# Optimization experiments

Measured on AMD Instinct MI355X. Metric: run time of the kernel, lower is better.

## Reference

```python
import jax, jax.numpy as jnp
import numpy as np

IMG = 8       # image_size
LH = 150      # l_h
LQ = 10       # l_q
K = 10        # value-iteration steps
B = 16384     # batch
N_STATES = 2 + IMG * IMG


def _conv(x, w, pad):
    # NCHW conv, stride 1
    return jax.lax.conv_general_dilated(
        x, w, window_strides=(1, 1), padding=[(pad, pad), (pad, pad)],
        dimension_numbers=('NCHW', 'OIHW', 'NCHW'))


def setup_inputs() -> dict:
    key = jax.random.key(0)
    ks = jax.random.split(key, 8)
    grid = jax.random.normal(ks[0], (B, IMG * IMG), dtype=jnp.float32)
    pos = jax.random.randint(ks[1], (B, 2), 0, IMG).astype(jnp.float32)
    S = jnp.concatenate([grid, pos], axis=1)                      # [B, 66]
    Wh = jax.random.normal(ks[2], (LH, 1, 3, 3), jnp.float32) * 0.1
    bh = jnp.zeros((LH,), jnp.float32)
    Wr = jax.random.normal(ks[3], (1, LH, 1, 1), jnp.float32) * 0.1
    Wq = jax.random.normal(ks[4], (LQ, 1, 3, 3), jnp.float32) * 0.1
    w = jax.random.normal(ks[5], (LQ, 1, 3, 3), jnp.float32) * 0.1
    Wfc = jax.random.normal(ks[6], (8, LQ), jnp.float32) * 0.1
    return {'S': S, 'Wh': Wh, 'bh': bh, 'Wr': Wr, 'Wq': Wq, 'w': w, 'Wfc': Wfc}


def reference(S, Wh, bh, Wr, Wq, w, Wfc):
    X = S[:, :IMG * IMG].reshape(-1, 1, IMG, IMG)                 # [B,1,8,8]
    s1 = S[:, IMG * IMG].astype(jnp.int32)                        # row index
    s2 = S[:, IMG * IMG + 1].astype(jnp.int32)                    # col index

    h = _conv(X, Wh, 1) + bh[None, :, None, None]                 # [B,150,8,8]
    r = _conv(h, Wr, 0)                                           # [B,1,8,8]
    q = _conv(r, Wq, 1)                                           # [B,10,8,8]
    v = jnp.max(q, axis=1, keepdims=True)                         # [B,1,8,8]

    Wcat = jnp.concatenate([Wq, w], axis=1)                       # [10,2,3,3]

    def step(v, _):
        qq = _conv(jnp.concatenate([r, v], axis=1), Wcat, 1)
        return jnp.max(qq, axis=1, keepdims=True), None

    v, _ = jax.lax.scan(step, v, None, length=K - 1)
    q = _conv(jnp.concatenate([r, v], axis=1), Wcat, 1)           # [B,10,8,8]

    bidx = jnp.arange(q.shape[0])
    q_sel = q[bidx, :, s1, s2]                                    # [B,10]
    logits = q_sel @ Wfc.T                                        # [B,8]
    return logits
```

## Files before the change

### kernel.cpp

```cpp
#include <hip/hip_runtime.h>

#define IMG 8
#define LH 150
#define LQ 10
#define KITER 10
#define ROW (IMG * IMG + 2)

__device__ __forceinline__ float bperm(int byte_addr, float v) {
    return __builtin_bit_cast(float,
        __builtin_amdgcn_ds_bpermute(byte_addr, __builtin_bit_cast(int, v)));
}

__device__ __forceinline__ float rfl(float v) {
    return __builtin_bit_cast(float,
        __builtin_amdgcn_readfirstlane(__builtin_bit_cast(int, v)));
}

__device__ __forceinline__ float swz24(float v) {
    return __builtin_bit_cast(float,
        __builtin_amdgcn_ds_swizzle(__builtin_bit_cast(int, v), 0x601F));
}

template <int CTRL>
__device__ __forceinline__ float dppf(float v) {
    return __builtin_bit_cast(float,
        __builtin_amdgcn_update_dpp(0, __builtin_bit_cast(int, v),
                                    CTRL, 0xF, 0xF, true));
}
#define DPP_SHR1 0x111
#define DPP_SHL1 0x101
#define DPP_SHR8 0x118
#define DPP_SHL8 0x108

__global__ __launch_bounds__(256, 8) void vin_kernel(
    const float* __restrict__ S,
    const float* __restrict__ Wh,
    const float* __restrict__ bh,
    const float* __restrict__ Wr,
    const float* __restrict__ Wq,
    const float* __restrict__ w,
    const float* __restrict__ Wfc,
    float* __restrict__ out,
    int B) {
    const int wave = threadIdx.x >> 6;
    const int lane = threadIdx.x & 63;
    const long b0 = (long)(blockIdx.x * 4 + wave) * 2;
    if (b0 >= B) return;

    const int item = lane >> 5;
    const int l32  = lane & 31;
    const int h    = l32 >> 4;
    const int q    = (l32 >> 3) & 1;
    const int x    = l32 & 7;

    const float mskL = (x > 0) ? 1.f : 0.f;
    const float mskR = (x < 7) ? 1.f : 0.f;
    const float m3   = (h == 1 && q == 0) ? 1.f : 0.f;
    const float m4   = (h == 0 && q == 1) ? 1.f : 0.f;

    float p[10];
    #pragma unroll
    for (int t = 0; t < 10; ++t) p[t] = 0.f;
    for (int c = lane; c < LH; c += 64) {
        const float wr = Wr[c];
        #pragma unroll
        for (int t = 0; t < 9; ++t) p[t] = fmaf(wr, Wh[c * 9 + t], p[t]);
        p[9] = fmaf(wr, bh[c], p[9]);
    }
    #pragma unroll
    for (int t = 0; t < 10; ++t)
        #pragma unroll
        for (int off = 32; off > 0; off >>= 1)
            p[t] += __shfl_xor(p[t], off);

    const long b = b0 + item;
    const float* Sb = S + b * ROW;
    float v[2];
    v[0] = Sb[(h * 4 + q) * 8 + x];
    v[1] = Sb[(h * 4 + 2 + q) * 8 + x];
    const int s1i = (int)Sb[IMG * IMG];
    const int s2i = (int)Sb[IMG * IMG + 1];
    const int selAddr = ((item << 5) + ((s1i >> 2) << 4) + ((s1i & 1) << 3) + s2i) << 2;
    const float e0 = (((s1i >> 1) & 1) == 0) ? 1.f : 0.f;
    const float e1 = 1.f - e0;

    auto rows5 = [&](const float vv[2], float d[5]) {
        const float X3 = swz24(vv[1]);
        const float X4 = swz24(vv[0]);
        d[1] = vv[0];
        d[3] = vv[1];
        d[2] = dppf<DPP_SHL8>(vv[0]) + dppf<DPP_SHR8>(vv[1]);
        d[0] = fmaf(X3, m3, dppf<DPP_SHR8>(vv[0]));
        d[4] = fmaf(X4, m4, dppf<DPP_SHL8>(vv[1]));
    };
    auto lcr = [&](const float d[5], float L[5], float R[5]) {
        #pragma unroll
        for (int j = 0; j < 5; ++j) {
            L[j] = mskL * dppf<DPP_SHR1>(d[j]);
            R[j] = mskR * dppf<DPP_SHL1>(d[j]);
        }
    };

    {
        float d[5], L[5], R[5];
        rows5(v, d); lcr(d, L, R);
        const float bias = p[9];
        #pragma unroll
        for (int r = 0; r < 2; ++r) {
            float a = bias;
            #pragma unroll
            for (int ky = 0; ky < 3; ++ky) {
                const int j = 2 * r + ky;
                a = fmaf(L[j], p[ky * 3 + 0], a);
                a = fmaf(d[j], p[ky * 3 + 1], a);
                a = fmaf(R[j], p[ky * 3 + 2], a);
            }
            v[r] = a;
        }
    }

    float qr[LQ][2];
    {
        float d[5], L[5], R[5];
        rows5(v, d); lcr(d, L, R);
        #pragma unroll
        for (int o = 0; o < LQ; ++o)
            #pragma unroll
            for (int r = 0; r < 2; ++r) {
                float a = L[2 * r] * Wq[o * 9 + 0];
                a = fmaf(d[2 * r],     Wq[o * 9 + 1], a);
                a = fmaf(R[2 * r],     Wq[o * 9 + 2], a);
                a = fmaf(L[2 * r + 1], Wq[o * 9 + 3], a);
                a = fmaf(d[2 * r + 1], Wq[o * 9 + 4], a);
                a = fmaf(R[2 * r + 1], Wq[o * 9 + 5], a);
                a = fmaf(L[2 * r + 2], Wq[o * 9 + 6], a);
                a = fmaf(d[2 * r + 2], Wq[o * 9 + 7], a);
                a = fmaf(R[2 * r + 2], Wq[o * 9 + 8], a);
                qr[o][r] = a;
            }
    }

    float wu[LQ][9];
    #pragma unroll
    for (int o = 0; o < LQ; ++o)
        #pragma unroll
        for (int t = 0; t < 9; ++t)
            wu[o][t] = rfl(w[o * 9 + t]);

    #pragma unroll
    for (int r = 0; r < 2; ++r) {
        const float g0 = fmaxf(fmaxf(qr[0][r], qr[1][r]), qr[2][r]);
        const float g1 = fmaxf(fmaxf(qr[3][r], qr[4][r]), qr[5][r]);
        const float g2 = fmaxf(fmaxf(qr[6][r], qr[7][r]), qr[8][r]);
        v[r] = fmaxf(fmaxf(g0, g1), fmaxf(g2, qr[9][r]));
    }

    #pragma unroll 1
    for (int k = 0; k < KITER - 1; ++k) {
        float d[5], L[5], R[5];
        rows5(v, d); lcr(d, L, R);
        float m[2];
        #pragma unroll
        for (int o = 0; o < LQ; ++o)
            #pragma unroll
            for (int r = 0; r < 2; ++r) {
                float a = qr[o][r];
                a = fmaf(L[2 * r],     wu[o][0], a);
                a = fmaf(d[2 * r],     wu[o][1], a);
                a = fmaf(R[2 * r],     wu[o][2], a);
                a = fmaf(L[2 * r + 1], wu[o][3], a);
                a = fmaf(d[2 * r + 1], wu[o][4], a);
                a = fmaf(R[2 * r + 1], wu[o][5], a);
                a = fmaf(L[2 * r + 2], wu[o][6], a);
                a = fmaf(d[2 * r + 2], wu[o][7], a);
                a = fmaf(R[2 * r + 2], wu[o][8], a);
                m[r] = (o == 0) ? a : fmaxf(m[r], a);
            }
        v[0] = m[0]; v[1] = m[1];
    }

    const int row = l32 & 7;
    float osum = 0.f;
    {
        float d[5], L[5], R[5];
        rows5(v, d); lcr(d, L, R);
        #pragma unroll
        for (int o = 0; o < LQ; ++o) {
            float a0, a1;
            #pragma unroll
            for (int r = 0; r < 2; ++r) {
                float a = qr[o][r];
                a = fmaf(L[2 * r],     wu[o][0], a);
                a = fmaf(d[2 * r],     wu[o][1], a);
                a = fmaf(R[2 * r],     wu[o][2], a);
                a = fmaf(L[2 * r + 1], wu[o][3], a);
                a = fmaf(d[2 * r + 1], wu[o][4], a);
                a = fmaf(R[2 * r + 1], wu[o][5], a);
                a = fmaf(L[2 * r + 2], wu[o][6], a);
                a = fmaf(d[2 * r + 2], wu[o][7], a);
                a = fmaf(R[2 * r + 2], wu[o][8], a);
                if (r == 0) a0 = a; else a1 = a;
            }
            float t = a0 * e0;
            t = fmaf(a1, e1, t);
            const float qs = bperm(selAddr, t);
            osum = fmaf(qs, Wfc[row * LQ + o], osum);
        }
    }
    if (l32 < 8) out[b * 8 + row] = osum;
}

extern "C" void kernel_launch(void* const* d_in, const int* in_sizes, int n_in,
                              void* d_out, int out_size, void* d_ws, size_t ws_size,
                              hipStream_t stream) {
    const float* S   = (const float*)d_in[0];
    const float* Wh  = (const float*)d_in[1];
    const float* bh  = (const float*)d_in[2];
    const float* Wr  = (const float*)d_in[3];
    const float* Wq  = (const float*)d_in[4];
    const float* w   = (const float*)d_in[5];
    const float* Wfc = (const float*)d_in[6];
    float* out = (float*)d_out;
    (void)d_ws; (void)ws_size;

    const int B = in_sizes[0] / ROW;

    const int grid = (B + 7) / 8;
    vin_kernel<<<grid, 256, 0, stream>>>(S, Wh, bh, Wr, Wq, w, Wfc, out, B);
}
```

Baseline: 110.6 us.

## Precompute collapsed Wr·Wh weights in a separate kernel and unroll VI loop

Moves the per-wave reduction of Wr against Wh and bh into a one-block pre-kernel that writes ten effective weights to the workspace. The main kernel then reads these from global memory instead of redoing 150-channel loads and shuffle reductions in every wave. It also lowers the launch-bounds occupancy hint from 8 to 6 and unrolls the value-iteration loop by 3. The cost is an extra kernel launch and a dependency between the two kernels, plus higher register pressure from the unroll.

```diff
diff --git a/kernel.cpp b/kernel.cpp
--- a/kernel.cpp
+++ b/kernel.cpp
@@ -32,14 +32,29 @@
 #define DPP_SHR8 0x118
 #define DPP_SHL8 0x108
 
-__global__ __launch_bounds__(256, 8) void vin_kernel(
+__global__ void weff_kernel(const float* __restrict__ Wh,
+                            const float* __restrict__ bh,
+                            const float* __restrict__ Wr,
+                            float* __restrict__ ws) {
+    const int wv = threadIdx.x >> 6;
+    const int lane = threadIdx.x & 63;
+    float partial = 0.f;
+    for (int c = lane; c < LH; c += 64) {
+        const float wr = Wr[c];
+        partial += wr * ((wv < 9) ? Wh[c * 9 + wv] : bh[c]);
+    }
+    #pragma unroll
+    for (int off = 32; off > 0; off >>= 1)
+        partial += __shfl_xor(partial, off);
+    if (lane == 0) ws[wv] = partial;
+}
+
+__global__ __launch_bounds__(256, 6) void vin_kernel(
     const float* __restrict__ S,
-    const float* __restrict__ Wh,
-    const float* __restrict__ bh,
-    const float* __restrict__ Wr,
     const float* __restrict__ Wq,
     const float* __restrict__ w,
     const float* __restrict__ Wfc,
+    const float* __restrict__ ws,
     float* __restrict__ out,
     int B) {
     const int wave = threadIdx.x >> 6;
@@ -57,21 +72,6 @@
     const float mskR = (x < 7) ? 1.f : 0.f;
     const float m3   = (h == 1 && q == 0) ? 1.f : 0.f;
     const float m4   = (h == 0 && q == 1) ? 1.f : 0.f;
-
-    float p[10];
-    #pragma unroll
-    for (int t = 0; t < 10; ++t) p[t] = 0.f;
-    for (int c = lane; c < LH; c += 64) {
-        const float wr = Wr[c];
-        #pragma unroll
-        for (int t = 0; t < 9; ++t) p[t] = fmaf(wr, Wh[c * 9 + t], p[t]);
-        p[9] = fmaf(wr, bh[c], p[9]);
-    }
-    #pragma unroll
-    for (int t = 0; t < 10; ++t)
-        #pragma unroll
-        for (int off = 32; off > 0; off >>= 1)
-            p[t] += __shfl_xor(p[t], off);
 
     const long b = b0 + item;
     const float* Sb = S + b * ROW;
@@ -104,16 +104,16 @@
     {
         float d[5], L[5], R[5];
         rows5(v, d); lcr(d, L, R);
-        const float bias = p[9];
+        const float bias = ws[9];
         #pragma unroll
         for (int r = 0; r < 2; ++r) {
             float a = bias;
             #pragma unroll
             for (int ky = 0; ky < 3; ++ky) {
                 const int j = 2 * r + ky;
-                a = fmaf(L[j], p[ky * 3 + 0], a);
-                a = fmaf(d[j], p[ky * 3 + 1], a);
-                a = fmaf(R[j], p[ky * 3 + 2], a);
+                a = fmaf(L[j], ws[ky * 3 + 0], a);
+                a = fmaf(d[j], ws[ky * 3 + 1], a);
+                a = fmaf(R[j], ws[ky * 3 + 2], a);
             }
             v[r] = a;
         }
@@ -155,7 +155,7 @@
         v[r] = fmaxf(fmaxf(g0, g1), fmaxf(g2, qr[9][r]));
     }
 
-    #pragma unroll 1
+    #pragma unroll 3
     for (int k = 0; k < KITER - 1; ++k) {
         float d[5], L[5], R[5];
         rows5(v, d); lcr(d, L, R);
@@ -221,10 +221,12 @@
     const float* w   = (const float*)d_in[5];
     const float* Wfc = (const float*)d_in[6];
     float* out = (float*)d_out;
-    (void)d_ws; (void)ws_size;
+    float* ws  = (float*)d_ws;
 
     const int B = in_sizes[0] / ROW;
 
+    weff_kernel<<<1, 640, 0, stream>>>(Wh, bh, Wr, ws);
+
     const int grid = (B + 7) / 8;
-    vin_kernel<<<grid, 256, 0, stream>>>(S, Wh, bh, Wr, Wq, w, Wfc, out, B);
-}
+    vin_kernel<<<grid, 256, 0, stream>>>(S, Wq, w, Wfc, ws, out, B);
+}
```

Measured after the change: 100.4 us. 9.2% less time.

## Split fused weight reduction across waves via LDS and tree-max the Q channels

Applied to the files above, without the earlier changes.

The fused conv-weight reduction (Wr·Wh and Wr·bh) was computed redundantly by every wave. It is now split across the four waves, each reducing 2-3 taps and publishing them through shared memory with a block barrier. The value-iteration loop is also unrolled by 3 and uses a tree of fmax instead of a serial max chain. The position loads are deferred until after the loop. These changes cut redundant global loads and shuffle reductions and shorten the dependency chain, at the cost of a __syncthreads, a lower occupancy hint (7 instead of 8) and possibly more register pressure.

```diff
diff --git a/kernel.cpp b/kernel.cpp
--- a/kernel.cpp
+++ b/kernel.cpp
@@ -32,7 +32,7 @@
 #define DPP_SHR8 0x118
 #define DPP_SHL8 0x108
 
-__global__ __launch_bounds__(256, 8) void vin_kernel(
+__global__ __launch_bounds__(256, 7) void vin_kernel(
     const float* __restrict__ S,
     const float* __restrict__ Wh,
     const float* __restrict__ bh,
@@ -44,6 +44,33 @@
     int B) {
     const int wave = threadIdx.x >> 6;
     const int lane = threadIdx.x & 63;
+
+    __shared__ float wsh[10];
+    {
+        const int nt    = (wave < 2) ? 3 : 2;
+        const int tbase = (wave < 2) ? wave * 3 : 6 + (wave - 2) * 2;
+        float p[3] = {0.f, 0.f, 0.f};
+        for (int c = lane; c < LH; c += 64) {
+            const float wr = Wr[c];
+            #pragma unroll
+            for (int j = 0; j < 3; ++j)
+                if (j < nt) {
+                    const int t = tbase + j;
+                    p[j] = fmaf(wr, (t < 9) ? Wh[c * 9 + t] : bh[c], p[j]);
+                }
+        }
+        #pragma unroll
+        for (int j = 0; j < 3; ++j)
+            if (j < nt) {
+                float pj = p[j];
+                #pragma unroll
+                for (int off = 32; off > 0; off >>= 1)
+                    pj += __shfl_xor(pj, off);
+                if (lane == 0) wsh[tbase + j] = pj;
+            }
+    }
+    __syncthreads();
+
     const long b0 = (long)(blockIdx.x * 4 + wave) * 2;
     if (b0 >= B) return;
 
@@ -58,31 +85,14 @@
     const float m3   = (h == 1 && q == 0) ? 1.f : 0.f;
     const float m4   = (h == 0 && q == 1) ? 1.f : 0.f;
 
-    float p[10];
-    #pragma unroll
-    for (int t = 0; t < 10; ++t) p[t] = 0.f;
-    for (int c = lane; c < LH; c += 64) {
-        const float wr = Wr[c];
-        #pragma unroll
-        for (int t = 0; t < 9; ++t) p[t] = fmaf(wr, Wh[c * 9 + t], p[t]);
-        p[9] = fmaf(wr, bh[c], p[9]);
-    }
-    #pragma unroll
-    for (int t = 0; t < 10; ++t)
-        #pragma unroll
-        for (int off = 32; off > 0; off >>= 1)
-            p[t] += __shfl_xor(p[t], off);
-
-    const long b = b0 + item;
-    const float* Sb = S + b * ROW;
+    const float* Sb = S + (b0 + item) * ROW;
     float v[2];
     v[0] = Sb[(h * 4 + q) * 8 + x];
     v[1] = Sb[(h * 4 + 2 + q) * 8 + x];
-    const int s1i = (int)Sb[IMG * IMG];
-    const int s2i = (int)Sb[IMG * IMG + 1];
-    const int selAddr = ((item << 5) + ((s1i >> 2) << 4) + ((s1i & 1) << 3) + s2i) << 2;
-    const float e0 = (((s1i >> 1) & 1) == 0) ? 1.f : 0.f;
-    const float e1 = 1.f - e0;
+
+    float wsr[10];
+    #pragma unroll
+    for (int t = 0; t < 10; ++t) wsr[t] = wsh[t];
 
     auto rows5 = [&](const float vv[2], float d[5]) {
         const float X3 = swz24(vv[1]);
@@ -104,16 +114,16 @@
     {
         float d[5], L[5], R[5];
         rows5(v, d); lcr(d, L, R);
-        const float bias = p[9];
+        const float bias = wsr[9];
         #pragma unroll
         for (int r = 0; r < 2; ++r) {
             float a = bias;
             #pragma unroll
             for (int ky = 0; ky < 3; ++ky) {
                 const int j = 2 * r + ky;
-                a = fmaf(L[j], p[ky * 3 + 0], a);
-                a = fmaf(d[j], p[ky * 3 + 1], a);
-                a = fmaf(R[j], p[ky * 3 + 2], a);
+                a = fmaf(L[j], wsr[ky * 3 + 0], a);
+                a = fmaf(d[j], wsr[ky * 3 + 1], a);
+                a = fmaf(R[j], wsr[ky * 3 + 2], a);
             }
             v[r] = a;
         }
@@ -155,30 +165,47 @@
         v[r] = fmaxf(fmaxf(g0, g1), fmaxf(g2, qr[9][r]));
     }
 
-    #pragma unroll 1
+    auto chan = [&](const float d[5], const float L[5], const float R[5],
+                    int o, int r) {
+        float a = qr[o][r];
+        a = fmaf(L[2 * r],     wu[o][0], a);
+        a = fmaf(d[2 * r],     wu[o][1], a);
+        a = fmaf(R[2 * r],     wu[o][2], a);
+        a = fmaf(L[2 * r + 1], wu[o][3], a);
+        a = fmaf(d[2 * r + 1], wu[o][4], a);
+        a = fmaf(R[2 * r + 1], wu[o][5], a);
+        a = fmaf(L[2 * r + 2], wu[o][6], a);
+        a = fmaf(d[2 * r + 2], wu[o][7], a);
+        a = fmaf(R[2 * r + 2], wu[o][8], a);
+        return a;
+    };
+
+    #pragma unroll 3
     for (int k = 0; k < KITER - 1; ++k) {
         float d[5], L[5], R[5];
         rows5(v, d); lcr(d, L, R);
-        float m[2];
-        #pragma unroll
-        for (int o = 0; o < LQ; ++o)
-            #pragma unroll
-            for (int r = 0; r < 2; ++r) {
-                float a = qr[o][r];
-                a = fmaf(L[2 * r],     wu[o][0], a);
-                a = fmaf(d[2 * r],     wu[o][1], a);
-                a = fmaf(R[2 * r],     wu[o][2], a);
-                a = fmaf(L[2 * r + 1], wu[o][3], a);
-                a = fmaf(d[2 * r + 1], wu[o][4], a);
-                a = fmaf(R[2 * r + 1], wu[o][5], a);
-                a = fmaf(L[2 * r + 2], wu[o][6], a);
-                a = fmaf(d[2 * r + 2], wu[o][7], a);
-                a = fmaf(R[2 * r + 2], wu[o][8], a);
-                m[r] = (o == 0) ? a : fmaxf(m[r], a);
-            }
-        v[0] = m[0]; v[1] = m[1];
-    }
-
+        #pragma unroll
+        for (int r = 0; r < 2; ++r) {
+            const float g0 = fmaxf(fmaxf(chan(d, L, R, 0, r),
+                                         chan(d, L, R, 1, r)),
+                                   chan(d, L, R, 2, r));
+            const float g1 = fmaxf(fmaxf(chan(d, L, R, 3, r),
+                                         chan(d, L, R, 4, r)),
+                                   chan(d, L, R, 5, r));
+            const float g2 = fmaxf(fmaxf(chan(d, L, R, 6, r),
+                                         chan(d, L, R, 7, r)),
+                                   chan(d, L, R, 8, r));
+            v[r] = fmaxf(fmaxf(g0, g1), fmaxf(g2, chan(d, L, R, 9, r)));
+        }
+    }
+
+    const long b = b0 + item;
+    const float* Sb2 = S + b * ROW;
+    const int s1i = (int)Sb2[IMG * IMG];
+    const int s2i = (int)Sb2[IMG * IMG + 1];
+    const int selAddr = ((item << 5) + ((s1i >> 2) << 4) + ((s1i & 1) << 3) + s2i) << 2;
+    const float e0 = (((s1i >> 1) & 1) == 0) ? 1.f : 0.f;
+    const float e1 = 1.f - e0;
     const int row = l32 & 7;
     float osum = 0.f;
     {
@@ -186,21 +213,8 @@
         rows5(v, d); lcr(d, L, R);
         #pragma unroll
         for (int o = 0; o < LQ; ++o) {
-            float a0, a1;
-            #pragma unroll
-            for (int r = 0; r < 2; ++r) {
-                float a = qr[o][r];
-                a = fmaf(L[2 * r],     wu[o][0], a);
-                a = fmaf(d[2 * r],     wu[o][1], a);
-                a = fmaf(R[2 * r],     wu[o][2], a);
-                a = fmaf(L[2 * r + 1], wu[o][3], a);
-                a = fmaf(d[2 * r + 1], wu[o][4], a);
-                a = fmaf(R[2 * r + 1], wu[o][5], a);
-                a = fmaf(L[2 * r + 2], wu[o][6], a);
-                a = fmaf(d[2 * r + 2], wu[o][7], a);
-                a = fmaf(R[2 * r + 2], wu[o][8], a);
-                if (r == 0) a0 = a; else a1 = a;
-            }
+            const float a0 = chan(d, L, R, o, 0);
+            const float a1 = chan(d, L, R, o, 1);
             float t = a0 * e0;
             t = fmaf(a1, e1, t);
             const float qs = bperm(selAddr, t);
```

Measured after the change: 122.4 us. +10.7%, slower.
